# Kernel tuning notes

Measured on AMD Instinct MI355X. Metric: run time of the kernel, lower is better.

## Reference

```python
import jax, jax.numpy as jnp
import numpy as np

EPS = 1e-8       # epsilon added to abs-diff in compute_sim
LN_EPS = 1e-5    # torch nn.LayerNorm default eps
NUM_HEADS = 8


def _layernorm(x, g, b):
    mu = jnp.mean(x, axis=-1, keepdims=True)
    var = jnp.mean((x - mu) ** 2, axis=-1, keepdims=True)
    return (x - mu) / jnp.sqrt(var + LN_EPS) * g + b


def _fla(x, alphas, betas):
    # x: [B, D]; alphas/betas: [H, 3] scalars per (head, {query,key,value})
    D = x.shape[-1]
    scale = 1.0 / jnp.sqrt(jnp.float32(D))
    acc = jnp.zeros_like(x)
    for h in range(alphas.shape[0]):  # small fixed head count; avoids H*B*D*D blowup
        q = alphas[h, 0] * x + betas[h, 0]
        k = alphas[h, 1] * x + betas[h, 1]
        v = alphas[h, 2] * x + betas[h, 2]
        # sim[b,i,j] = 1/(|q[b,j]-k[b,i]|+eps), softmax over j, scaled by 1/sqrt(D)
        sim = jax.nn.softmax(1.0 / (jnp.abs(q[:, None, :] - k[:, :, None]) + EPS), axis=-1) * scale
        acc = acc + jnp.einsum('bij,bj->bi', sim, v)
    return x + acc


def setup_inputs() -> dict:
    key = jax.random.key(0)
    ks = jax.random.split(key, 8)
    B, D, L = 1024, 256, 2  # batch, feature dim (input_dim == hidden dims), num hidden layers
    x = jax.random.normal(ks[0], (B, D), dtype=jnp.float32)
    fla_alphas = jax.random.uniform(ks[1], (L, NUM_HEADS, 3), dtype=jnp.float32)
    fla_betas = jax.random.uniform(ks[2], (L, NUM_HEADS, 3), dtype=jnp.float32)
    lim = 1.0 / np.sqrt(D)
    lin_W = jax.random.uniform(ks[3], (L, D, D), dtype=jnp.float32, minval=-lim, maxval=lim)
    lin_b = jax.random.uniform(ks[4], (L, D), dtype=jnp.float32, minval=-lim, maxval=lim)
    fla_ln_g = jnp.ones((L, D), jnp.float32)
    fla_ln_b = jnp.zeros((L, D), jnp.float32)
    lin_ln_g = jnp.ones((L, D), jnp.float32)
    lin_ln_b = jnp.zeros((L, D), jnp.float32)
    out_W = jax.random.uniform(ks[5], (D, 1), dtype=jnp.float32, minval=-lim, maxval=lim)
    out_b = jax.random.uniform(ks[6], (1,), dtype=jnp.float32, minval=-lim, maxval=lim)
    return dict(x=x, fla_alphas=fla_alphas, fla_betas=fla_betas,
                fla_ln_g=fla_ln_g, fla_ln_b=fla_ln_b,
                lin_W=lin_W, lin_b=lin_b,
                lin_ln_g=lin_ln_g, lin_ln_b=lin_ln_b,
                out_W=out_W, out_b=out_b)


def reference(x, fla_alphas, fla_betas, fla_ln_g, fla_ln_b,
              lin_W, lin_b, lin_ln_g, lin_ln_b, out_W, out_b):
    L = fla_alphas.shape[0]
    for i in range(L):
        x = _fla(x, fla_alphas[i], fla_betas[i])
        x = jax.nn.relu(x)
        x = _layernorm(x, fla_ln_g[i], fla_ln_b[i])
        x = x @ lin_W[i] + lin_b[i]
        x = jax.nn.relu(x)
        x = _layernorm(x, lin_ln_g[i], lin_ln_b[i])
    return x @ out_W + out_b
```

## Files before the change

### kernel.cpp

```cpp
#include <hip/hip_runtime.h>

#define DD 256
#define NH 8

constexpr float LN_EPS = 1e-5f;
constexpr float SCALE  = 0.0625f;
constexpr float KS     = 8.2629579e-8f;
constexpr float A_EXP  = 12102203.0f;
constexpr float B_EXP  = 1064986816.0f;
#define RCP_MAGIC 0x7EF311C3u

__device__ __forceinline__ float wexp_ys(float yabs, float w, float Bh) {
    float f = fmaf(yabs, w, Bh);
    unsigned u;
    asm("v_cvt_u32_f32 %0, %1" : "=v"(u) : "v"(f));
    return __uint_as_float(u);
}

__device__ __forceinline__ float2 block_reduce2(float a, float b, float* sc, int tid) {
    #pragma unroll
    for (int off = 32; off; off >>= 1) {
        a += __shfl_down(a, off, 64);
        b += __shfl_down(b, off, 64);
    }
    __syncthreads();
    if ((tid & 63) == 0) { int w = tid >> 6; sc[2*w] = a; sc[2*w+1] = b; }
    __syncthreads();
    float ra = 0.f, rb = 0.f;
    #pragma unroll
    for (int w = 0; w < 8; ++w) { ra += sc[2*w]; rb += sc[2*w+1]; }
    return make_float2(ra, rb);
}

template<int LAST>
__global__ __launch_bounds__(512, 8) void flann_layer(
    const float* __restrict__ x_in,
    const float* __restrict__ alphas,
    const float* __restrict__ betas,
    const float* __restrict__ g1, const float* __restrict__ b1,
    const float* __restrict__ W,  const float* __restrict__ wb,
    const float* __restrict__ g2, const float* __restrict__ b2,
    const float* __restrict__ outW, const float* __restrict__ outB,
    float* __restrict__ out)
{
    __shared__ __align__(16) float xs[DD];
    __shared__ __align__(16) float xln[DD];
    __shared__ float combE[2][NH][DD];
    __shared__ float combW[2][NH][DD];
    __shared__ float sc[16];

    const int tid  = threadIdx.x;
    const int i    = tid & (DD - 1);
    const int half = tid >> 8;
    const int bidx = blockIdx.x;

    float xv = x_in[bidx * DD + i];
    if (half == 0) xs[i] = xv * KS;
    __syncthreads();

    const float4* xs4 = reinterpret_cast<const float4*>(xs);
    const int jb = half * (DD / 8);

    float aqv[NH], cv[NH], dmn[NH], Bv[NH];
    #pragma unroll
    for (int h = 0; h < NH; ++h) {
        const float aq = alphas[h*3+0], ak = alphas[h*3+1];
        const float bq = betas [h*3+0], bk = betas [h*3+1];
        aqv[h] = aq;
        cv[h]  = (bq - fmaf(ak, xv, bk)) * KS;
        dmn[h] = 1e38f;
    }

    #pragma unroll 4
    for (int j4 = 0; j4 < DD/8; ++j4) {
        float4 xj = xs4[jb + j4];
        #pragma unroll
        for (int h = 0; h < NH; ++h) {
            float d0 = fmaf(aqv[h], xj.x, cv[h]);
            float d1 = fmaf(aqv[h], xj.y, cv[h]);
            float d2 = fmaf(aqv[h], xj.z, cv[h]);
            float d3 = fmaf(aqv[h], xj.w, cv[h]);
            dmn[h] = fminf(dmn[h], fminf(fabsf(d0), fabsf(d1)));
            dmn[h] = fminf(dmn[h], fminf(fabsf(d2), fabsf(d3)));
        }
    }
    #pragma unroll
    for (int h = 0; h < NH; ++h) combE[half][h][i] = dmn[h];
    __syncthreads();
    #pragma unroll
    for (int h = 0; h < NH; ++h) {
        float dm = fminf(dmn[h], combE[half ^ 1][h][i]);
        float y  = __uint_as_float(RCP_MAGIC - __float_as_uint(dm));
        float w  = fmaf(-dm, fabsf(y), 2.0f);
        Bv[h]    = B_EXP - fabsf(y) * w;
    }
    __syncthreads();

    float sE[NH], sW[NH];
    #pragma unroll
    for (int h = 0; h < NH; ++h) { sE[h] = 0.f; sW[h] = 0.f; }

    #pragma unroll 4
    for (int j4 = 0; j4 < DD/8; ++j4) {
        float4 xj = xs4[jb + j4];
        #pragma unroll
        for (int h = 0; h < NH; ++h) {
            const float aq = aqv[h], c = cv[h], Bh = Bv[h];
            float dh0 = fmaf(aq, xj.x, c);
            float dh1 = fmaf(aq, xj.y, c);
            float dh2 = fmaf(aq, xj.z, c);
            float dh3 = fmaf(aq, xj.w, c);
            float y0 = __uint_as_float(RCP_MAGIC - __float_as_uint(dh0));
            float y1 = __uint_as_float(RCP_MAGIC - __float_as_uint(dh1));
            float y2 = __uint_as_float(RCP_MAGIC - __float_as_uint(dh2));
            float y3 = __uint_as_float(RCP_MAGIC - __float_as_uint(dh3));
            float w0 = fmaf(-fabsf(dh0), fabsf(y0), 2.0f);
            float w1 = fmaf(-fabsf(dh1), fabsf(y1), 2.0f);
            float w2 = fmaf(-fabsf(dh2), fabsf(y2), 2.0f);
            float w3 = fmaf(-fabsf(dh3), fabsf(y3), 2.0f);
            float e0 = wexp_ys(fabsf(y0), w0, Bh);
            float e1 = wexp_ys(fabsf(y1), w1, Bh);
            float e2 = wexp_ys(fabsf(y2), w2, Bh);
            float e3 = wexp_ys(fabsf(y3), w3, Bh);
            sE[h] += e0; sW[h] = fmaf(e0, xj.x, sW[h]);
            sE[h] += e1; sW[h] = fmaf(e1, xj.y, sW[h]);
            sE[h] += e2; sW[h] = fmaf(e2, xj.z, sW[h]);
            sE[h] += e3; sW[h] = fmaf(e3, xj.w, sW[h]);
        }
    }
    #pragma unroll
    for (int h = 0; h < NH; ++h) { combE[half][h][i] = sE[h]; combW[half][h][i] = sW[h]; }
    __syncthreads();

    float xr = 0.f;
    if (half == 0) {
        float acc = 0.f;
        #pragma unroll
        for (int h = 0; h < NH; ++h) {
            const float av = alphas[h*3+2], bv = betas[h*3+2];
            float sEt = sE[h] + combE[1][h][i];
            float sWt = (sW[h] + combW[1][h][i]) * A_EXP;
            acc += fmaf(av, sWt, bv * sEt) * __builtin_amdgcn_rcpf(sEt);
        }
        xr = fmaxf(fmaf(SCALE, acc, xv), 0.f);
    }

    float2 r = block_reduce2(xr, xr * xr, sc, tid);
    float mu  = r.x * (1.f / DD);
    float var = r.y * (1.f / DD) - mu * mu;
    if (half == 0) {
        float xn = (xr - mu) * __builtin_amdgcn_rsqf(var + LN_EPS);
        xln[i] = fmaf(xn, g1[i], b1[i]);
    }
    __syncthreads();

    const float4* xl4 = reinterpret_cast<const float4*>(xln);
    float ga0 = (half == 0) ? wb[i] : 0.f, ga1 = 0.f, ga2 = 0.f, ga3 = 0.f;
    #pragma unroll 8
    for (int d4 = 0; d4 < DD/8; ++d4) {
        float4 xd = xl4[jb + d4];
        int dr = 4 * (jb + d4);
        ga0 = fmaf(xd.x, W[(dr + 0) * DD + i], ga0);
        ga1 = fmaf(xd.y, W[(dr + 1) * DD + i], ga1);
        ga2 = fmaf(xd.z, W[(dr + 2) * DD + i], ga2);
        ga3 = fmaf(xd.w, W[(dr + 3) * DD + i], ga3);
    }
    combE[half][0][i] = (ga0 + ga1) + (ga2 + ga3);
    __syncthreads();

    float gv = 0.f;
    if (half == 0) gv = fmaxf(combE[0][0][i] + combE[1][0][i], 0.f);

    r = block_reduce2(gv, gv * gv, sc, tid);
    mu  = r.x * (1.f / DD);
    var = r.y * (1.f / DD) - mu * mu;
    float xo = 0.f;
    if (half == 0)
        xo = fmaf((gv - mu) * __builtin_amdgcn_rsqf(var + LN_EPS), g2[i], b2[i]);

    if (!LAST) {
        if (half == 0) out[bidx * DD + i] = xo;
    } else {
        float pr = (half == 0) ? xo * outW[i] : 0.f;
        float2 p = block_reduce2(pr, 0.f, sc, tid);
        if (tid == 0) out[bidx] = p.x + outB[0];
    }
}

extern "C" void kernel_launch(void* const* d_in, const int* in_sizes, int n_in,
                              void* d_out, int out_size, void* d_ws, size_t ws_size,
                              hipStream_t stream) {
    const float* x      = (const float*)d_in[0];
    const float* alphas = (const float*)d_in[1];
    const float* betas  = (const float*)d_in[2];
    const float* flag   = (const float*)d_in[3];
    const float* flab   = (const float*)d_in[4];
    const float* linW   = (const float*)d_in[5];
    const float* linb   = (const float*)d_in[6];
    const float* ling   = (const float*)d_in[7];
    const float* linb2  = (const float*)d_in[8];
    const float* outW   = (const float*)d_in[9];
    const float* outB   = (const float*)d_in[10];

    const int B = in_sizes[0] / DD;
    float* ws   = (float*)d_ws;
    float* outp = (float*)d_out;

    dim3 grid(B), block(512);
    flann_layer<0><<<grid, block, 0, stream>>>(
        x, alphas, betas, flag, flab, linW, linb, ling, linb2,
        nullptr, nullptr, ws);
    flann_layer<1><<<grid, block, 0, stream>>>(
        ws, alphas + NH*3, betas + NH*3, flag + DD, flab + DD,
        linW + DD*DD, linb + DD, ling + DD, linb2 + DD,
        outW, outB, outp);
}
```

Before: 187.4 us.

## Split heads across thread groups instead of splitting j-range across halves

Blocks grow from 512 to 1024 threads, and each 256-thread group now handles 2 of the 8 heads over the full j range instead of all 8 heads over half the j range. Each head's min and softmax sums are therefore complete within one thread, so the cross-half min exchange, one barrier and the large combE/combW shared buffers go away. Per-head outputs are combined through a small 4x256 shared array, and the block reduction reads its partials as float4. The cost is doubled block size, with higher register pressure and scheduling constraints per block, and the GEMV is now split four ways.

```diff
diff --git a/kernel.cpp b/kernel.cpp
--- a/kernel.cpp
+++ b/kernel.cpp
@@ -2,6 +2,8 @@
 
 #define DD 256
 #define NH 8
+#define HPT 2
+#define NHG 4
 
 constexpr float LN_EPS = 1e-5f;
 constexpr float SCALE  = 0.0625f;
@@ -24,16 +26,20 @@
         b += __shfl_down(b, off, 64);
     }
     __syncthreads();
-    if ((tid & 63) == 0) { int w = tid >> 6; sc[2*w] = a; sc[2*w+1] = b; }
-    __syncthreads();
-    float ra = 0.f, rb = 0.f;
-    #pragma unroll
-    for (int w = 0; w < 8; ++w) { ra += sc[2*w]; rb += sc[2*w+1]; }
+    if ((tid & 63) == 0) { int w = tid >> 6; sc[w] = a; sc[16 + w] = b; }
+    __syncthreads();
+    const float4* s4 = reinterpret_cast<const float4*>(sc);
+    float4 a0 = s4[0], a1 = s4[1], a2 = s4[2], a3 = s4[3];
+    float4 b0 = s4[4], b1 = s4[5], b2 = s4[6], b3 = s4[7];
+    float ra = ((a0.x+a0.y)+(a0.z+a0.w)) + ((a1.x+a1.y)+(a1.z+a1.w))
+             + ((a2.x+a2.y)+(a2.z+a2.w)) + ((a3.x+a3.y)+(a3.z+a3.w));
+    float rb = ((b0.x+b0.y)+(b0.z+b0.w)) + ((b1.x+b1.y)+(b1.z+b1.w))
+             + ((b2.x+b2.y)+(b2.z+b2.w)) + ((b3.x+b3.y)+(b3.z+b3.w));
     return make_float2(ra, rb);
 }
 
 template<int LAST>
-__global__ __launch_bounds__(512, 8) void flann_layer(
+__global__ __launch_bounds__(1024, 8) void flann_layer(
     const float* __restrict__ x_in,
     const float* __restrict__ alphas,
     const float* __restrict__ betas,
@@ -45,67 +51,62 @@
 {
     __shared__ __align__(16) float xs[DD];
     __shared__ __align__(16) float xln[DD];
-    __shared__ float combE[2][NH][DD];
-    __shared__ float combW[2][NH][DD];
-    __shared__ float sc[16];
+    __shared__ float comb[NHG][DD];
+    __shared__ float sc[32];
 
     const int tid  = threadIdx.x;
     const int i    = tid & (DD - 1);
-    const int half = tid >> 8;
+    const int hg   = tid >> 8;
     const int bidx = blockIdx.x;
 
     float xv = x_in[bidx * DD + i];
-    if (half == 0) xs[i] = xv * KS;
+    if (hg == 0) xs[i] = xv * KS;
     __syncthreads();
 
     const float4* xs4 = reinterpret_cast<const float4*>(xs);
-    const int jb = half * (DD / 8);
-
-    float aqv[NH], cv[NH], dmn[NH], Bv[NH];
-    #pragma unroll
-    for (int h = 0; h < NH; ++h) {
+
+    float aqv[HPT], cv[HPT], dmn[HPT], Bv[HPT];
+    #pragma unroll
+    for (int hh = 0; hh < HPT; ++hh) {
+        const int h = hg * HPT + hh;
         const float aq = alphas[h*3+0], ak = alphas[h*3+1];
         const float bq = betas [h*3+0], bk = betas [h*3+1];
-        aqv[h] = aq;
-        cv[h]  = (bq - fmaf(ak, xv, bk)) * KS;
-        dmn[h] = 1e38f;
+        aqv[hh] = aq;
+        cv[hh]  = (bq - fmaf(ak, xv, bk)) * KS;
+        dmn[hh] = 1e38f;
     }
 
     #pragma unroll 4
-    for (int j4 = 0; j4 < DD/8; ++j4) {
-        float4 xj = xs4[jb + j4];
+    for (int j4 = 0; j4 < DD/4; ++j4) {
+        float4 xj = xs4[j4];
         #pragma unroll
-        for (int h = 0; h < NH; ++h) {
-            float d0 = fmaf(aqv[h], xj.x, cv[h]);
-            float d1 = fmaf(aqv[h], xj.y, cv[h]);
-            float d2 = fmaf(aqv[h], xj.z, cv[h]);
-            float d3 = fmaf(aqv[h], xj.w, cv[h]);
-            dmn[h] = fminf(dmn[h], fminf(fabsf(d0), fabsf(d1)));
-            dmn[h] = fminf(dmn[h], fminf(fabsf(d2), fabsf(d3)));
+        for (int hh = 0; hh < HPT; ++hh) {
+            float d0 = fmaf(aqv[hh], xj.x, cv[hh]);
+            float d1 = fmaf(aqv[hh], xj.y, cv[hh]);
+            float d2 = fmaf(aqv[hh], xj.z, cv[hh]);
+            float d3 = fmaf(aqv[hh], xj.w, cv[hh]);
+            dmn[hh] = fminf(dmn[hh], fminf(fabsf(d0), fabsf(d1)));
+            dmn[hh] = fminf(dmn[hh], fminf(fabsf(d2), fabsf(d3)));
         }
     }
     #pragma unroll
-    for (int h = 0; h < NH; ++h) combE[half][h][i] = dmn[h];
-    __syncthreads();
-    #pragma unroll
-    for (int h = 0; h < NH; ++h) {
-        float dm = fminf(dmn[h], combE[half ^ 1][h][i]);
+    for (int hh = 0; hh < HPT; ++hh) {
+        float dm = dmn[hh];
         float y  = __uint_as_float(RCP_MAGIC - __float_as_uint(dm));
         float w  = fmaf(-dm, fabsf(y), 2.0f);
-        Bv[h]    = B_EXP - fabsf(y) * w;
-    }
-    __syncthreads();
-
-    float sE[NH], sW[NH];
-    #pragma unroll
-    for (int h = 0; h < NH; ++h) { sE[h] = 0.f; sW[h] = 0.f; }
+        Bv[hh]   = B_EXP - fabsf(y) * w;
+    }
+
+    float sE[HPT], sW[HPT];
+    #pragma unroll
+    for (int hh = 0; hh < HPT; ++hh) { sE[hh] = 0.f; sW[hh] = 0.f; }
 
     #pragma unroll 4
-    for (int j4 = 0; j4 < DD/8; ++j4) {
-        float4 xj = xs4[jb + j4];
+    for (int j4 = 0; j4 < DD/4; ++j4) {
+        float4 xj = xs4[j4];
         #pragma unroll
-        for (int h = 0; h < NH; ++h) {
-            const float aq = aqv[h], c = cv[h], Bh = Bv[h];
+        for (int hh = 0; hh < HPT; ++hh) {
+            const float aq = aqv[hh], c = cv[hh], Bh = Bv[hh];
             float dh0 = fmaf(aq, xj.x, c);
             float dh1 = fmaf(aq, xj.y, c);
             float dh2 = fmaf(aq, xj.z, c);
@@ -122,66 +123,69 @@
             float e1 = wexp_ys(fabsf(y1), w1, Bh);
             float e2 = wexp_ys(fabsf(y2), w2, Bh);
             float e3 = wexp_ys(fabsf(y3), w3, Bh);
-            sE[h] += e0; sW[h] = fmaf(e0, xj.x, sW[h]);
-            sE[h] += e1; sW[h] = fmaf(e1, xj.y, sW[h]);
-            sE[h] += e2; sW[h] = fmaf(e2, xj.z, sW[h]);
-            sE[h] += e3; sW[h] = fmaf(e3, xj.w, sW[h]);
+            sE[hh] += e0; sW[hh] = fmaf(e0, xj.x, sW[hh]);
+            sE[hh] += e1; sW[hh] = fmaf(e1, xj.y, sW[hh]);
+            sE[hh] += e2; sW[hh] = fmaf(e2, xj.z, sW[hh]);
+            sE[hh] += e3; sW[hh] = fmaf(e3, xj.w, sW[hh]);
         }
     }
-    #pragma unroll
-    for (int h = 0; h < NH; ++h) { combE[half][h][i] = sE[h]; combW[half][h][i] = sW[h]; }
+
+    float accp = 0.f;
+    #pragma unroll
+    for (int hh = 0; hh < HPT; ++hh) {
+        const int h = hg * HPT + hh;
+        const float av = alphas[h*3+2], bv = betas[h*3+2];
+        float sWt = sW[hh] * A_EXP;
+        accp += fmaf(av, sWt, bv * sE[hh]) * __builtin_amdgcn_rcpf(sE[hh]);
+    }
+    comb[hg][i] = accp;
     __syncthreads();
 
     float xr = 0.f;
-    if (half == 0) {
-        float acc = 0.f;
-        #pragma unroll
-        for (int h = 0; h < NH; ++h) {
-            const float av = alphas[h*3+2], bv = betas[h*3+2];
-            float sEt = sE[h] + combE[1][h][i];
-            float sWt = (sW[h] + combW[1][h][i]) * A_EXP;
-            acc += fmaf(av, sWt, bv * sEt) * __builtin_amdgcn_rcpf(sEt);
-        }
+    if (hg == 0) {
+        float acc = (comb[0][i] + comb[1][i]) + (comb[2][i] + comb[3][i]);
         xr = fmaxf(fmaf(SCALE, acc, xv), 0.f);
     }
 
     float2 r = block_reduce2(xr, xr * xr, sc, tid);
     float mu  = r.x * (1.f / DD);
     float var = r.y * (1.f / DD) - mu * mu;
-    if (half == 0) {
+    if (hg == 0) {
         float xn = (xr - mu) * __builtin_amdgcn_rsqf(var + LN_EPS);
         xln[i] = fmaf(xn, g1[i], b1[i]);
     }
     __syncthreads();
 
     const float4* xl4 = reinterpret_cast<const float4*>(xln);
-    float ga0 = (half == 0) ? wb[i] : 0.f, ga1 = 0.f, ga2 = 0.f, ga3 = 0.f;
+    float ga0 = (hg == 0) ? wb[i] : 0.f, ga1 = 0.f, ga2 = 0.f, ga3 = 0.f;
     #pragma unroll 8
-    for (int d4 = 0; d4 < DD/8; ++d4) {
-        float4 xd = xl4[jb + d4];
-        int dr = 4 * (jb + d4);
+    for (int d4 = 0; d4 < DD/16; ++d4) {
+        int g4 = hg * (DD/16) + d4;
+        float4 xd = xl4[g4];
+        int dr = 4 * g4;
         ga0 = fmaf(xd.x, W[(dr + 0) * DD + i], ga0);
         ga1 = fmaf(xd.y, W[(dr + 1) * DD + i], ga1);
         ga2 = fmaf(xd.z, W[(dr + 2) * DD + i], ga2);
         ga3 = fmaf(xd.w, W[(dr + 3) * DD + i], ga3);
     }
-    combE[half][0][i] = (ga0 + ga1) + (ga2 + ga3);
+    comb[hg][i] = (ga0 + ga1) + (ga2 + ga3);
     __syncthreads();
 
     float gv = 0.f;
-    if (half == 0) gv = fmaxf(combE[0][0][i] + combE[1][0][i], 0.f);
+    if (hg == 0)
+        gv = fmaxf((comb[0][i] + comb[1][i]) + (comb[2][i] + comb[3][i]), 0.f);
 
     r = block_reduce2(gv, gv * gv, sc, tid);
     mu  = r.x * (1.f / DD);
     var = r.y * (1.f / DD) - mu * mu;
     float xo = 0.f;
-    if (half == 0)
+    if (hg == 0)
         xo = fmaf((gv - mu) * __builtin_amdgcn_rsqf(var + LN_EPS), g2[i], b2[i]);
 
     if (!LAST) {
-        if (half == 0) out[bidx * DD + i] = xo;
+        if (hg == 0) out[bidx * DD + i] = xo;
     } else {
-        float pr = (half == 0) ? xo * outW[i] : 0.f;
+        float pr = (hg == 0) ? xo * outW[i] : 0.f;
         float2 p = block_reduce2(pr, 0.f, sc, tid);
         if (tid == 0) out[bidx] = p.x + outB[0];
     }
@@ -206,7 +210,7 @@
     float* ws   = (float*)d_ws;
     float* outp = (float*)d_out;
 
-    dim3 grid(B), block(512);
+    dim3 grid(B), block(1024);
     flann_layer<0><<<grid, block, 0, stream>>>(
         x, alphas, betas, flag, flab, linW, linb, ling, linb2,
         nullptr, nullptr, ws);
```

After: 190.0 us. No clear change (+1.3%).
